# Optimization experiments

Hardware: AMD Instinct MI355X
Metric: run time of the kernel (lower is better)

## Reference

```python
import jax, jax.numpy as jnp
import numpy as np
import math

QUERY_SIZE = 128
KEY_SIZE = 128
VALUE_SIZE = 64
ATTN_SIZE = 64
NQ = 4096
NK = 8192


def setup_inputs() -> dict:
    key = jax.random.key(0)
    ks = jax.random.split(key, 9)
    scale_q = 1.0 / math.sqrt(QUERY_SIZE)
    scale_k = 1.0 / math.sqrt(KEY_SIZE)
    scale_v = 1.0 / math.sqrt(VALUE_SIZE)
    return {
        "q": jax.random.normal(ks[0], (NQ, QUERY_SIZE), jnp.float32),
        "k": jax.random.normal(ks[1], (NK, KEY_SIZE), jnp.float32),
        "v": jax.random.normal(ks[2], (NK, VALUE_SIZE), jnp.float32),
        # nn.Linear weights: [out_features, in_features], y = x W^T + b
        "Wq": jax.random.uniform(ks[3], (ATTN_SIZE, QUERY_SIZE), jnp.float32, -scale_q, scale_q),
        "bq": jax.random.uniform(ks[4], (ATTN_SIZE,), jnp.float32, -scale_q, scale_q),
        "Wk": jax.random.uniform(ks[5], (ATTN_SIZE, KEY_SIZE), jnp.float32, -scale_k, scale_k),
        "bk": jax.random.uniform(ks[6], (ATTN_SIZE,), jnp.float32, -scale_k, scale_k),
        "Wv": jax.random.uniform(ks[7], (VALUE_SIZE, VALUE_SIZE), jnp.float32, -scale_v, scale_v),
        "bv": jax.random.uniform(ks[8], (VALUE_SIZE,), jnp.float32, -scale_v, scale_v),
    }


def reference(q, k, v, Wq, bq, Wk, bk, Wv, bv):
    # Linear projections (y = x W^T + b)
    query = q @ Wq.T + bq          # [Nq, A]
    key_p = k @ Wk.T + bk          # [Nk, A]
    value = v @ Wv.T + bv          # [Nk, Dv]
    # scaled dot-product scores
    g = (query @ key_p.T) / math.sqrt(ATTN_SIZE)   # [Nq, Nk]
    score = jax.nn.softmax(g, axis=-1)
    # sum(score[...,None] * value, axis=-2) == score @ value
    output = score @ value          # [Nq, Dv]
    return output
```

## Files before the change

kernel.cpp:

```cpp
#include <hip/hip_runtime.h>
#include <hip/hip_bf16.h>

typedef __bf16 bf16;
typedef __bf16 bf16x4 __attribute__((ext_vector_type(4)));
typedef __bf16 bf16x8 __attribute__((ext_vector_type(8)));
typedef float floatx4 __attribute__((ext_vector_type(4)));

#define MFMA16(A, B, C) __builtin_amdgcn_mfma_f32_16x16x32_bf16(A, B, C, 0, 0, 0)

constexpr int NQ = 4096;
constexpr int NK = 8192;
constexpr int AD = 64;
constexpr int KSPLIT = 32;
constexpr int BQ = 128;
constexpr int BK = 64;
constexpr int KPB = NK / KSPLIT;
constexpr int TILES = KPB / BK;
constexpr float QSCALE = 0.125f * 1.4426950408889634f;

__device__ inline bf16x8 ld_cvt8(const float* __restrict__ p) {
  float4 a = *(const float4*)p;
  float4 b = *(const float4*)(p + 4);
  bf16x8 r = {(bf16)a.x, (bf16)a.y, (bf16)a.z, (bf16)a.w,
              (bf16)b.x, (bf16)b.y, (bf16)b.z, (bf16)b.w};
  return r;
}

__global__ __launch_bounds__(256) void proj_mfma(
    const float* __restrict__ q, const float* __restrict__ k,
    const float* __restrict__ v,
    const float* __restrict__ Wq, const float* __restrict__ bq,
    const float* __restrict__ Wk, const float* __restrict__ bk,
    const float* __restrict__ Wv, const float* __restrict__ bv,
    bf16* __restrict__ qout, bf16* __restrict__ kout, bf16* __restrict__ vtout) {
  const int tid = threadIdx.x;
  const int wave = tid >> 6, lane = tid & 63;
  const int l16 = lane & 15, quad = lane >> 4;
  const int b = blockIdx.x;

  if (b < 192) {
    const bool isQ = (b < 64);
    const float* X = isQ ? q : k;
    const float* W = isQ ? Wq : Wk;
    const float* bias = isQ ? bq : bk;
    bf16* Y = isQ ? qout : kout;
    const float oscale = isQ ? QSCALE : 1.0f;
    const int rowbase = (isQ ? b : b - 64) * 64 + wave * 16;

    bf16x8 bf_[4];
#pragma unroll
    for (int ks = 0; ks < 4; ++ks)
      bf_[ks] = ld_cvt8(X + (size_t)(rowbase + l16) * 128 + ks * 32 + quad * 8);
    bf16x8 af[4][4];
#pragma unroll
    for (int mt = 0; mt < 4; ++mt)
#pragma unroll
      for (int ks = 0; ks < 4; ++ks)
        af[mt][ks] = ld_cvt8(W + (size_t)(mt * 16 + l16) * 128 + ks * 32 + quad * 8);

    floatx4 acc[4];
#pragma unroll
    for (int mt = 0; mt < 4; ++mt) acc[mt] = (floatx4){0.f, 0.f, 0.f, 0.f};
#pragma unroll
    for (int mt = 0; mt < 4; ++mt)
#pragma unroll
      for (int ks = 0; ks < 4; ++ks)
        acc[mt] = MFMA16(af[mt][ks], bf_[ks], acc[mt]);

#pragma unroll
    for (int mt = 0; mt < 4; ++mt) {
      float4 bb = *(const float4*)(bias + mt * 16 + quad * 4);
      bf16x4 o = {(bf16)((acc[mt][0] + bb.x) * oscale),
                  (bf16)((acc[mt][1] + bb.y) * oscale),
                  (bf16)((acc[mt][2] + bb.z) * oscale),
                  (bf16)((acc[mt][3] + bb.w) * oscale)};
      *(bf16x4*)(Y + (size_t)(rowbase + l16) * 64 + mt * 16 + quad * 4) = o;
    }
  } else {
    const int keybase = (b - 192) * 64 + wave * 16;
    bf16x8 af2[2];
#pragma unroll
    for (int ks = 0; ks < 2; ++ks)
      af2[ks] = ld_cvt8(v + (size_t)(keybase + l16) * 64 + ks * 32 + quad * 8);
    bf16x8 bf2[4][2];
#pragma unroll
    for (int nt = 0; nt < 4; ++nt)
#pragma unroll
      for (int ks = 0; ks < 2; ++ks)
        bf2[nt][ks] = ld_cvt8(Wv + (size_t)(nt * 16 + l16) * 64 + ks * 32 + quad * 8);

    floatx4 acc[4];
#pragma unroll
    for (int nt = 0; nt < 4; ++nt) acc[nt] = (floatx4){0.f, 0.f, 0.f, 0.f};
#pragma unroll
    for (int nt = 0; nt < 4; ++nt)
#pragma unroll
      for (int ks = 0; ks < 2; ++ks)
        acc[nt] = MFMA16(af2[ks], bf2[nt][ks], acc[nt]);

#pragma unroll
    for (int nt = 0; nt < 4; ++nt) {
      float bvv = bv[nt * 16 + l16];
      bf16x4 o = {(bf16)(acc[nt][0] + bvv), (bf16)(acc[nt][1] + bvv),
                  (bf16)(acc[nt][2] + bvv), (bf16)(acc[nt][3] + bvv)};
      *(bf16x4*)(vtout + (size_t)(nt * 16 + l16) * NK + keybase + quad * 4) = o;
    }
  }
}

__global__ __launch_bounds__(256, 4) void flash_kernel(
    const bf16* __restrict__ qp, const bf16* __restrict__ kp,
    const bf16* __restrict__ vt, bf16* __restrict__ Opart,
    float* __restrict__ lpart) {
  __shared__ __align__(16) bf16 Pt[4][32][72];

  const int tid = threadIdx.x;
  const int wave = tid >> 6;
  const int lane = tid & 63;
  const int l16 = lane & 15;
  const int quad = lane >> 4;
  const int ks = blockIdx.x;
  const int qb = blockIdx.y;
  const int qbase = qb * BQ + wave * 32;

  bf16x8 qf[2][2];
#pragma unroll
  for (int g = 0; g < 2; ++g)
#pragma unroll
    for (int c = 0; c < 2; ++c)
      qf[g][c] = *(const bf16x8*)(qp + (size_t)(qbase + g * 16 + l16) * AD +
                                  c * 32 + quad * 8);

  floatx4 o[2][4];
#pragma unroll
  for (int g = 0; g < 2; ++g)
#pragma unroll
    for (int nt = 0; nt < 4; ++nt)
      o[g][nt] = (floatx4){0.f, 0.f, 0.f, 0.f};
  float lsum[2] = {0.f, 0.f};

  for (int kt = 0; kt < TILES; ++kt) {
    const int keybase = ks * KPB + kt * BK;

#pragma unroll
    for (int st = 0; st < 4; ++st) {
      const bf16* krow = kp + (size_t)(keybase + st * 16 + l16) * AD + quad * 8;
      bf16x8 ka0 = *(const bf16x8*)krow;
      bf16x8 ka1 = *(const bf16x8*)(krow + 32);
#pragma unroll
      for (int g = 0; g < 2; ++g) {
        floatx4 acc = {0.f, 0.f, 0.f, 0.f};
        acc = MFMA16(ka0, qf[g][0], acc);
        acc = MFMA16(ka1, qf[g][1], acc);
        float p0 = __builtin_amdgcn_exp2f(acc[0]);
        float p1 = __builtin_amdgcn_exp2f(acc[1]);
        float p2 = __builtin_amdgcn_exp2f(acc[2]);
        float p3 = __builtin_amdgcn_exp2f(acc[3]);
        lsum[g] += (p0 + p1) + (p2 + p3);
        bf16x4 pk = {(bf16)p0, (bf16)p1, (bf16)p2, (bf16)p3};
        *(bf16x4*)&Pt[wave][g * 16 + l16][st * 16 + quad * 4] = pk;
      }
    }

    bf16x8 pf[2][2];
#pragma unroll
    for (int g = 0; g < 2; ++g)
#pragma unroll
      for (int c = 0; c < 2; ++c)
        pf[g][c] = *(const bf16x8*)&Pt[wave][g * 16 + l16][quad * 8 + c * 32];

#pragma unroll
    for (int nt = 0; nt < 4; ++nt) {
      const bf16* vrow = vt + (size_t)(nt * 16 + l16) * NK + keybase + quad * 8;
      bf16x8 vb0 = *(const bf16x8*)vrow;
      bf16x8 vb1 = *(const bf16x8*)(vrow + 32);
#pragma unroll
      for (int g = 0; g < 2; ++g) {
        o[g][nt] = MFMA16(pf[g][0], vb0, o[g][nt]);
        o[g][nt] = MFMA16(pf[g][1], vb1, o[g][nt]);
      }
    }
  }

#pragma unroll
  for (int g = 0; g < 2; ++g) {
    float t = lsum[g];
    t += __shfl_xor(t, 16, 64);
    t += __shfl_xor(t, 32, 64);
    lsum[g] = t;
  }

  bf16* ob = Opart + (size_t)ks * NQ * AD + (size_t)qbase * AD;
#pragma unroll
  for (int g = 0; g < 2; ++g)
#pragma unroll
    for (int nt = 0; nt < 4; ++nt)
#pragma unroll
      for (int r = 0; r < 4; ++r)
        ob[(size_t)(g * 16 + quad * 4 + r) * AD + nt * 16 + l16] =
            (bf16)o[g][nt][r];
  if (quad == 0) {
#pragma unroll
    for (int g = 0; g < 2; ++g)
      lpart[(size_t)ks * NQ + qbase + g * 16 + l16] = lsum[g];
  }
}

__global__ __launch_bounds__(256) void combine_kernel(
    const bf16* __restrict__ Opart, const float* __restrict__ lpart,
    float* __restrict__ out) {
  int t = blockIdx.x * 256 + threadIdx.x;
  int gid = t * 4;
  int qrow = gid >> 6;
  float ls = 0.f;
#pragma unroll
  for (int s = 0; s < KSPLIT; ++s) ls += lpart[(size_t)s * NQ + qrow];
  float a0 = 0.f, a1 = 0.f, a2 = 0.f, a3 = 0.f;
#pragma unroll
  for (int s = 0; s < KSPLIT; ++s) {
    bf16x4 ov = *(const bf16x4*)(Opart + (size_t)s * NQ * AD + gid);
    a0 += (float)ov[0];
    a1 += (float)ov[1];
    a2 += (float)ov[2];
    a3 += (float)ov[3];
  }
  float inv = 1.0f / ls;
  float4 res = {a0 * inv, a1 * inv, a2 * inv, a3 * inv};
  *(float4*)(out + gid) = res;
}

extern "C" void kernel_launch(void* const* d_in, const int* in_sizes, int n_in,
                              void* d_out, int out_size, void* d_ws,
                              size_t ws_size, hipStream_t stream) {
  const float* q = (const float*)d_in[0];
  const float* k = (const float*)d_in[1];
  const float* v = (const float*)d_in[2];
  const float* Wq = (const float*)d_in[3];
  const float* bq = (const float*)d_in[4];
  const float* Wk = (const float*)d_in[5];
  const float* bk = (const float*)d_in[6];
  const float* Wv = (const float*)d_in[7];
  const float* bv = (const float*)d_in[8];
  float* out = (float*)d_out;

  char* ws = (char*)d_ws;
  bf16* qout = (bf16*)(ws);
  bf16* kout = (bf16*)(ws + 524288);
  bf16* vtout = (bf16*)(ws + 1572864);
  bf16* Opart = (bf16*)(ws + 2621440);
  float* lpart = (float*)(ws + 2621440 + (size_t)KSPLIT * NQ * AD * 2);

  proj_mfma<<<320, 256, 0, stream>>>(q, k, v, Wq, bq, Wk, bk, Wv, bv, qout,
                                     kout, vtout);
  flash_kernel<<<dim3(KSPLIT, NQ / BQ), 256, 0, stream>>>(qout, kout, vtout,
                                                          Opart, lpart);
  combine_kernel<<<NQ * AD / 1024, 256, 0, stream>>>(Opart, lpart, out);
}
```

Baseline: 122.8 us.

## Stage K/V tiles through shared memory with register prefetch of next tile

```diff
diff --git a/kernel.cpp b/kernel.cpp
--- a/kernel.cpp
+++ b/kernel.cpp
@@ -112,6 +112,8 @@
     const bf16* __restrict__ qp, const bf16* __restrict__ kp,
     const bf16* __restrict__ vt, bf16* __restrict__ Opart,
     float* __restrict__ lpart) {
+  __shared__ __align__(16) bf16 Kt[BK][72];
+  __shared__ __align__(16) bf16 Vts[AD][72];
   __shared__ __align__(16) bf16 Pt[4][32][72];
 
   const int tid = threadIdx.x;
@@ -123,6 +125,8 @@
   const int qb = blockIdx.y;
   const int qbase = qb * BQ + wave * 32;
 
+  const int srow = tid >> 3, scg = tid & 7;
+
   bf16x8 qf[2][2];
 #pragma unroll
   for (int g = 0; g < 2; ++g)
@@ -139,14 +143,31 @@
       o[g][nt] = (floatx4){0.f, 0.f, 0.f, 0.f};
   float lsum[2] = {0.f, 0.f};
 
+  int kb0 = ks * KPB;
+  bf16x8 kpre0 = *(const bf16x8*)(kp + (size_t)(kb0 + srow) * AD + scg * 8);
+  bf16x8 kpre1 = *(const bf16x8*)(kp + (size_t)(kb0 + srow + 32) * AD + scg * 8);
+  bf16x8 vpre0 = *(const bf16x8*)(vt + (size_t)srow * NK + kb0 + scg * 8);
+  bf16x8 vpre1 = *(const bf16x8*)(vt + (size_t)(srow + 32) * NK + kb0 + scg * 8);
+
+#pragma unroll
   for (int kt = 0; kt < TILES; ++kt) {
     const int keybase = ks * KPB + kt * BK;
+    const int nb = ks * KPB + ((kt + 1) & (TILES - 1)) * BK;
+
+    __syncthreads();
+    *(bf16x8*)&Kt[srow][scg * 8] = kpre0;
+    *(bf16x8*)&Kt[srow + 32][scg * 8] = kpre1;
+    *(bf16x8*)&Vts[srow][scg * 8] = vpre0;
+    *(bf16x8*)&Vts[srow + 32][scg * 8] = vpre1;
+    __syncthreads();
+
+    kpre0 = *(const bf16x8*)(kp + (size_t)(nb + srow) * AD + scg * 8);
+    kpre1 = *(const bf16x8*)(kp + (size_t)(nb + srow + 32) * AD + scg * 8);
 
 #pragma unroll
     for (int st = 0; st < 4; ++st) {
-      const bf16* krow = kp + (size_t)(keybase + st * 16 + l16) * AD + quad * 8;
-      bf16x8 ka0 = *(const bf16x8*)krow;
-      bf16x8 ka1 = *(const bf16x8*)(krow + 32);
+      bf16x8 ka0 = *(const bf16x8*)&Kt[st * 16 + l16][quad * 8];
+      bf16x8 ka1 = *(const bf16x8*)&Kt[st * 16 + l16][quad * 8 + 32];
 #pragma unroll
       for (int g = 0; g < 2; ++g) {
         floatx4 acc = {0.f, 0.f, 0.f, 0.f};
@@ -162,6 +183,9 @@
       }
     }
 
+    vpre0 = *(const bf16x8*)(vt + (size_t)srow * NK + nb + scg * 8);
+    vpre1 = *(const bf16x8*)(vt + (size_t)(srow + 32) * NK + nb + scg * 8);
+
     bf16x8 pf[2][2];
 #pragma unroll
     for (int g = 0; g < 2; ++g)
@@ -171,9 +195,8 @@
 
 #pragma unroll
     for (int nt = 0; nt < 4; ++nt) {
-      const bf16* vrow = vt + (size_t)(nt * 16 + l16) * NK + keybase + quad * 8;
-      bf16x8 vb0 = *(const bf16x8*)vrow;
-      bf16x8 vb1 = *(const bf16x8*)(vrow + 32);
+      bf16x8 vb0 = *(const bf16x8*)&Vts[nt * 16 + l16][quad * 8];
+      bf16x8 vb1 = *(const bf16x8*)&Vts[nt * 16 + l16][quad * 8 + 32];
 #pragma unroll
       for (int g = 0; g < 2; ++g) {
         o[g][nt] = MFMA16(pf[g][0], vb0, o[g][nt]);
```

Result: faster. 104.6 us (-14.8%).
